# Kernel optimization log

Hardware: AMD Instinct MI355X
Metric: run time of the kernel (lower is better)

## Reference

```python
import jax, jax.numpy as jnp
import numpy as np

LOG_EPS = 1e-30
MIN_EPS = 1e-8
N_CLASS = 19
GAMMA = 1.0        # focal_gamma
ADAPT_B = 0.2
ADAPT_A = 0.9      # beta (a_decay == 0)
ADAPT_D = 8.0
CONF_THRESH = 0.8  # uda_confidence_thresh


def setup_inputs() -> dict:
    key = jax.random.key(0)
    k1, k2 = jax.random.split(key)
    N, C, H, W = 2, N_CLASS, 512, 1024
    logits_before = jax.random.normal(k1, (N, C, H, W), jnp.float32)
    logits_after = jax.random.normal(k2, (N, C, H, W), jnp.float32)
    cls_thresh = jnp.ones((N_CLASS,), jnp.float32) * CONF_THRESH
    return {"logits_before": logits_before, "logits_after": logits_after,
            "cls_thresh": cls_thresh}


def ias_thresh(conf, label, cls_thresh):
    # conf, label: [N,H,W] max-prob and argmax class per pixel
    conf_f = conf.reshape(-1)    # [T]
    label_f = label.reshape(-1)  # [T]

    def per_class(c, thr):
        # class-c confidences, others pushed to the end of the descending sort
        vals = jnp.where(label_f == c, conf_f, -jnp.inf)
        ext = jnp.concatenate([vals, thr[None]])  # append current threshold
        srt = -jnp.sort(-ext)                     # descending
        count = jnp.sum(label_f == c)
        # index = int(len_extend * adapt_b * thresh**adapt_d); len_extend = count+1
        idx = jnp.floor((count + 1).astype(jnp.float32) * ADAPT_B * thr ** ADAPT_D).astype(jnp.int32)
        return srt[idx]  # count==0 -> idx==0 -> picks thr (matches torch branch)

    return jax.vmap(per_class)(jnp.arange(N_CLASS), cls_thresh)


def reference(logits_before, logits_after, cls_thresh):
    pb = jax.nn.softmax(logits_before, axis=1)
    pa = jax.nn.softmax(logits_after, axis=1)
    pb_d = jax.lax.stop_gradient(pb)
    log_pb_d = jnp.log(pb_d + LOG_EPS)
    log_pa = jnp.log(pa + LOG_EPS)

    bma = 1.0 - pa  # focal_type == 1: ones_like(pb_d) - pa
    label = jnp.argmax(pb_d, axis=1)  # [N,H,W]
    conf = jnp.max(pb_d, axis=1)      # [N,H,W]
    # scatter(select_mask)+sum == gather the argmax channel
    sel_diff = jnp.take_along_axis(bma, label[:, None], axis=1)  # [N,1,H,W]

    loss_kldiv = pb_d * (log_pb_d - jnp.abs(sel_diff) ** GAMMA * log_pa)
    loss_entropy = -pb * jnp.log(pb + LOG_EPS)
    loss = jnp.sum(loss_kldiv + loss_entropy, axis=1)  # [N,H,W]

    tmp = ias_thresh(conf, label, cls_thresh)
    new_thresh = ADAPT_A * cls_thresh + (1.0 - ADAPT_A) * tmp
    new_thresh = jnp.where(new_thresh >= 1.0, 0.999, new_thresh)

    pix_thresh = new_thresh[label]           # [N,H,W]
    mask = conf > pix_thresh
    adapt_ratio = jnp.mean(mask.astype(jnp.float32))
    solid_ratio = jnp.mean((conf > CONF_THRESH).astype(jnp.float32))

    # loss[mask] -> clamp -> mean, expressed as a masked mean (jit-safe)
    num = jnp.sum(jnp.where(mask, jnp.maximum(loss, MIN_EPS), 0.0))
    den = jnp.maximum(jnp.sum(mask).astype(loss.dtype), 1.0)
    return num / den, adapt_ratio, solid_ratio
```

## Files before the change

### kernel.cpp

```cpp
#include <hip/hip_runtime.h>
#include <math.h>

#define NCLS 19
#define HW   (512*1024)
#define CHW  (NCLS*HW)
#define TPIX (2*HW)
#define NB   512
#define NPART 32
#define CAND_MAX 4096
#define SUBB 1024
#define SCAP 256

#define WS_PART   0
#define WS_CANDC  622592
#define WS_ACCUM  622720
#define WS_DONE   622784
#define WS_SEL    622848
#define WS_NEWTH  623360
#define WS_CONF   623616
#define WS_LOSS   4817920
#define WS_LABEL  9012224
#define WS_CAND   10060800

#define CH_STRIDE4 (HW/4)
__global__ __launch_bounds__(256, 4)
void k1_pixel(const float* __restrict__ lb_t, const float* __restrict__ la_t,
              float* __restrict__ conf_o, float* __restrict__ loss_o,
              unsigned char* __restrict__ label_o,
              unsigned int* __restrict__ cand_cnt,
              unsigned int* __restrict__ accum_u,
              unsigned int* __restrict__ done)
{
    const int tid = threadIdx.x;
    if (blockIdx.x == 0) {
        if (tid < NCLS)            cand_cnt[tid] = 0u;
        else if (tid < NCLS + 3)   accum_u[tid - NCLS] = 0u;
        else if (tid < NCLS + 5)   done[tid - NCLS - 3] = 0u;
    }
    const int g    = blockIdx.x * 256 + tid;
    const int pix0 = g << 2;
    const int n    = pix0 >> 19;
    const int rem  = pix0 & (HW - 1);
    const float4* bb = (const float4*)(lb_t + (size_t)n * CHW + rem);
    const float4* ab = (const float4*)(la_t + (size_t)n * CHW + rem);

    float mb[4], zb[4], dot[4], ma[4], za[4], a_lab[4];
    int lab[4];
#pragma unroll
    for (int j = 0; j < 4; ++j) {
        mb[j] = -INFINITY; ma[j] = -INFINITY;
        zb[j] = 0.0f; za[j] = 0.0f; dot[j] = 0.0f; a_lab[j] = 0.0f; lab[j] = -1;
    }

    float4 bA0, bA1, bA2, bA3, aA0, aA1, aA2, aA3;
    float4 bB0, bB1, bB2, bB3, aB0, aB1, aB2, aB3;

#define LOADA(c0, NC)                                                          \
    do {                                                                       \
        bA0 = bb[(size_t)(c0 + 0) * CH_STRIDE4];                               \
        aA0 = ab[(size_t)(c0 + 0) * CH_STRIDE4];                               \
        if (NC > 1) { bA1 = bb[(size_t)(c0 + 1) * CH_STRIDE4];                 \
                      aA1 = ab[(size_t)(c0 + 1) * CH_STRIDE4]; }               \
        if (NC > 2) { bA2 = bb[(size_t)(c0 + 2) * CH_STRIDE4];                 \
                      aA2 = ab[(size_t)(c0 + 2) * CH_STRIDE4]; }               \
        if (NC > 3) { bA3 = bb[(size_t)(c0 + 3) * CH_STRIDE4];                 \
                      aA3 = ab[(size_t)(c0 + 3) * CH_STRIDE4]; }               \
        __builtin_amdgcn_sched_barrier(0);                                     \
    } while (0)
#define LOADB(c0, NC)                                                          \
    do {                                                                       \
        bB0 = bb[(size_t)(c0 + 0) * CH_STRIDE4];                               \
        aB0 = ab[(size_t)(c0 + 0) * CH_STRIDE4];                               \
        if (NC > 1) { bB1 = bb[(size_t)(c0 + 1) * CH_STRIDE4];                 \
                      aB1 = ab[(size_t)(c0 + 1) * CH_STRIDE4]; }               \
        if (NC > 2) { bB2 = bb[(size_t)(c0 + 2) * CH_STRIDE4];                 \
                      aB2 = ab[(size_t)(c0 + 2) * CH_STRIDE4]; }               \
        if (NC > 3) { bB3 = bb[(size_t)(c0 + 3) * CH_STRIDE4];                 \
                      aB3 = ab[(size_t)(c0 + 3) * CH_STRIDE4]; }               \
        __builtin_amdgcn_sched_barrier(0);                                     \
    } while (0)

#define STEP(c, bv, av)                                                        \
    do {                                                                       \
        _Pragma("unroll")                                                      \
        for (int j = 0; j < 4; ++j) {                                          \
            float b = ((const float*)&(bv))[j];                                \
            float a = ((const float*)&(av))[j];                                \
            float mn = fmaxf(mb[j], b);                                        \
            float eo = __expf(mb[j] - mn);       \
            float en = __expf(b - mn);                                         \
            zb[j]  = zb[j] * eo + en;                                          \
            dot[j] = dot[j] * eo + en * a;                                     \
            bool upd = b > mb[j];               \
            lab[j]   = upd ? (c) : lab[j];                                     \
            a_lab[j] = upd ? a : a_lab[j];                                     \
            mb[j] = mn;                                                        \
            float mna = fmaxf(ma[j], a);                                       \
            za[j] = za[j] * __expf(ma[j] - mna) + __expf(a - mna);             \
            ma[j] = mna;                                                       \
        }                                                                      \
    } while (0)

    LOADA(0, 4);
    LOADB(4, 4);
    STEP(0, bA0, aA0); STEP(1, bA1, aA1); STEP(2, bA2, aA2); STEP(3, bA3, aA3);
    LOADA(8, 4);
    STEP(4, bB0, aB0); STEP(5, bB1, aB1); STEP(6, bB2, aB2); STEP(7, bB3, aB3);
    LOADB(12, 4);
    STEP(8, bA0, aA0); STEP(9, bA1, aA1); STEP(10, bA2, aA2); STEP(11, bA3, aA3);
    LOADA(16, 3);
    STEP(12, bB0, aB0); STEP(13, bB1, aB1); STEP(14, bB2, aB2); STEP(15, bB3, aB3);
    STEP(16, bA0, aA0); STEP(17, bA1, aA1); STEP(18, bA2, aA2);

    float4 cf4, ls4; uchar4 lb4;
#pragma unroll
    for (int j = 0; j < 4; ++j) {
        float cf = 1.0f / zb[j];
        float pa_lab = __expf(a_lab[j] - ma[j]) / za[j];
        float ls = (1.0f - pa_lab) * (ma[j] + __logf(za[j]) - dot[j] / zb[j]);
        ((float*)&cf4)[j] = cf;
        ((float*)&ls4)[j] = ls;
        ((unsigned char*)&lb4)[j] = (unsigned char)lab[j];
    }
    ((float4*)conf_o)[g] = cf4;
    ((float4*)loss_o)[g] = ls4;
    ((uchar4*)label_o)[g] = lb4;
#undef LOADA
#undef LOADB
#undef STEP
}

__global__ __launch_bounds__(512)
void k2_hist(const float4* __restrict__ conf, const uchar4* __restrict__ label,
             unsigned short* __restrict__ part)
{
    __shared__ unsigned int lh[NCLS * NB];
    const int t = threadIdx.x;
    for (int w = t; w < NCLS * NB; w += 512) lh[w] = 0u;
    __syncthreads();

    const int per4  = TPIX / 4 / NPART;
    const int base4 = blockIdx.x * per4;
    for (int i = 0; i < per4 / 512; ++i) {
        int g = base4 + i * 512 + t;
        float4 c4 = conf[g];
        uchar4 l4 = label[g];
        float cf[4] = {c4.x, c4.y, c4.z, c4.w};
        int   lb[4] = {l4.x, l4.y, l4.z, l4.w};
#pragma unroll
        for (int k = 0; k < 4; ++k) {
            int bin = (int)(cf[k] * (float)NB);
            bin = bin < (NB - 1) ? bin : (NB - 1);
            atomicAdd(&lh[lb[k] * NB + bin], 1u);
        }
    }
    __syncthreads();

    unsigned short* dst = part + blockIdx.x * (NCLS * NB);
    for (int w = t; w < NCLS * NB; w += 512) dst[w] = (unsigned short)lh[w];
}

__global__ __launch_bounds__(256)
void k2_select(const unsigned short* __restrict__ part, const float* __restrict__ cls_thresh,
               int* __restrict__ sel, unsigned int* __restrict__ cand_cnt,
               float* __restrict__ cand)
{
    int c = blockIdx.x;
    int t = threadIdx.x;
    float thr = cls_thresh[c];
    int thr_bin = (int)(thr * (float)NB); thr_bin = thr_bin < (NB-1) ? thr_bin : (NB-1);

    int base = NB - (t + 1) * 2;
    unsigned h0 = 0, h1 = 0;
#pragma unroll 8
    for (int b = 0; b < NPART; ++b) {
        const unsigned short* p = part + b * (NCLS * NB) + c * NB;
        h0 += p[base];
        h1 += p[base + 1];
    }
    if (base == thr_bin)     h0 += 1u;
    if (base + 1 == thr_bin) h1 += 1u;
    unsigned s = h0 + h1;

    __shared__ unsigned sc[256];
    sc[t] = s;
    __syncthreads();
    for (int off = 1; off < 256; off <<= 1) {
        unsigned vt = sc[t];
        unsigned vp = (t >= off) ? sc[t - off] : 0u;
        __syncthreads();
        sc[t] = vt + vp;
        __syncthreads();
    }
    unsigned total_ext = sc[255];
    unsigned cnt = total_ext - 1u;
    int idx = (int)floorf((float)(cnt + 1u) * 0.2f * powf(thr, 8.0f));

    unsigned above = sc[t] - s;
    if ((unsigned)idx >= above && (unsigned)idx < above + s) {
        int B, r;
        if ((unsigned)idx < above + h1) { B = base + 1; r = (int)((unsigned)idx - above); }
        else                            { B = base;     r = (int)((unsigned)idx - above - h1); }
        sel[2 * c]     = B;
        sel[2 * c + 1] = r;
        if (B == thr_bin) {
            unsigned pos = atomicAdd(&cand_cnt[c], 1u);
            if (pos < CAND_MAX) cand[c * CAND_MAX + pos] = thr;
        }
    }
}

__global__ __launch_bounds__(256)
void k3_gather(const float4* __restrict__ conf, const uchar4* __restrict__ label,
               const int* __restrict__ sel, unsigned int* __restrict__ cand_cnt,
               float* __restrict__ cand)
{
    int g = blockIdx.x * 256 + threadIdx.x;
    float4 c4 = conf[g];
    uchar4 l4 = label[g];
    float cf[4] = {c4.x, c4.y, c4.z, c4.w};
    int   lb[4] = {l4.x, l4.y, l4.z, l4.w};
#pragma unroll
    for (int i = 0; i < 4; ++i) {
        int bin = (int)(cf[i] * (float)NB);
        bin = bin < (NB - 1) ? bin : (NB - 1);
        if (bin == sel[2 * lb[i]]) {
            unsigned pos = atomicAdd(&cand_cnt[lb[i]], 1u);
            if (pos < CAND_MAX) cand[lb[i] * CAND_MAX + pos] = cf[i];
        }
    }
}

__global__ __launch_bounds__(256)
void k4_thresh(const int* __restrict__ sel, const unsigned int* __restrict__ cand_cnt,
               const float* __restrict__ cand, const float* __restrict__ cls_thresh,
               float* __restrict__ newth)
{
    __shared__ unsigned int subh[SUBB];
    __shared__ float        sbuf[SCAP];
    __shared__ unsigned int scnt;
    __shared__ int          sS;
    __shared__ unsigned int sR2;
    __shared__ float        sres;

    const int c = blockIdx.x;
    const int t = threadIdx.x;
    unsigned mc = cand_cnt[c];
    int m = (int)(mc < (unsigned)CAND_MAX ? mc : (unsigned)CAND_MAX);
    int B = sel[2 * c];
    int r = sel[2 * c + 1];
    const float* v = cand + c * CAND_MAX;
    const float scale = (float)NB;

    for (int i = t; i < SUBB; i += 256) subh[i] = 0u;
    if (t == 0) { scnt = 0u; sS = 0; sR2 = 0u; sres = 0.0f; }
    __syncthreads();

    for (int i = t; i < m; i += 256) {
        float x = v[i];
        int s = (int)((x * scale - (float)B) * (float)SUBB);
        s = s < 0 ? 0 : (s > SUBB - 1 ? SUBB - 1 : s);
        atomicAdd(&subh[s], 1u);
    }
    __syncthreads();

    if (t < 64) {
        int lane = t;
        int cb = SUBB - 16 * (lane + 1);
        unsigned hsum = 0;
        for (int i = 0; i < 16; ++i) hsum += subh[cb + i];
        unsigned incl = hsum;
        for (int off = 1; off < 64; off <<= 1) {
            unsigned q = __shfl_up(incl, off, 64);
            if (lane >= off) incl += q;
        }
        unsigned above = incl - hsum;
        if ((unsigned)r >= above && (unsigned)r < above + hsum) {
            unsigned cum = above;
            for (int i = 15; i >= 0; --i) {
                unsigned h = subh[cb + i];
                if ((unsigned)r < cum + h) { sS = cb + i; sR2 = (unsigned)r - cum; break; }
                cum += h;
            }
        }
    }
    __syncthreads();
    const int S = sS;
    const unsigned r2 = sR2;

    for (int i = t; i < m; i += 256) {
        float x = v[i];
        int s = (int)((x * scale - (float)B) * (float)SUBB);
        s = s < 0 ? 0 : (s > SUBB - 1 ? SUBB - 1 : s);
        if (s == S) {
            unsigned p = atomicAdd(&scnt, 1u);
            if (p < (unsigned)SCAP) sbuf[p] = x;
        }
    }
    __syncthreads();
    unsigned cntS = scnt;

    if (cntS <= (unsigned)SCAP) {
        for (int i = t; i < (int)cntS; i += 256) {
            float x = sbuf[i];
            int gc = 0, e = 0;
            for (int j = 0; j < (int)cntS; ++j) {
                float y = sbuf[j];
                gc += (y > x); e += (y == x);
            }
            if (gc <= (int)r2 && (int)r2 < gc + e) sres = x;
        }
    } else {
        for (int i = t; i < m; i += 256) {
            float x = v[i];
            int s = (int)((x * scale - (float)B) * (float)SUBB);
            s = s < 0 ? 0 : (s > SUBB - 1 ? SUBB - 1 : s);
            if (s != S) continue;
            int gc = 0, e = 0;
            for (int j = 0; j < m; ++j) {
                float y = v[j];
                int sj = (int)((y * scale - (float)B) * (float)SUBB);
                sj = sj < 0 ? 0 : (sj > SUBB - 1 ? SUBB - 1 : sj);
                if (sj != S) continue;
                gc += (y > x); e += (y == x);
            }
            if (gc <= (int)r2 && (int)r2 < gc + e) sres = x;
        }
    }
    __syncthreads();
    if (t == 0) {
        float thr = cls_thresh[c];
        float nt = 0.9f * thr + 0.1f * sres;
        if (nt >= 1.0f) nt = 0.999f;
        newth[c] = nt;
    }
}

__global__ __launch_bounds__(256)
void k5_reduce_out(const float4* __restrict__ conf, const float4* __restrict__ loss,
                   const uchar4* __restrict__ label, const float* __restrict__ newth,
                   float* __restrict__ accum, unsigned int* __restrict__ done,
                   float* __restrict__ out)
{
    __shared__ float th[NCLS];
    if (threadIdx.x < NCLS) th[threadIdx.x] = newth[threadIdx.x];
    __syncthreads();

    int g = blockIdx.x * 256 + threadIdx.x;
    float4 c4 = conf[g];
    float4 s4 = loss[g];
    uchar4 l4 = label[g];
    float cf[4] = {c4.x, c4.y, c4.z, c4.w};
    float lv[4] = {s4.x, s4.y, s4.z, s4.w};
    int   lb[4] = {l4.x, l4.y, l4.z, l4.w};

    float ls = 0.0f; int mask = 0, solid = 0;
#pragma unroll
    for (int i = 0; i < 4; ++i) {
        bool m = cf[i] > th[lb[i]];
        mask  += m ? 1 : 0;
        solid += (cf[i] > 0.8f) ? 1 : 0;
        ls    += m ? fmaxf(lv[i], 1e-8f) : 0.0f;
    }
    for (int off = 32; off > 0; off >>= 1) {
        ls    += __shfl_down(ls, off, 64);
        mask  += __shfl_down(mask, off, 64);
        solid += __shfl_down(solid, off, 64);
    }
    __shared__ float s_ls[4];
    __shared__ int   s_m[4], s_s[4];
    int w = threadIdx.x >> 6;
    if ((threadIdx.x & 63) == 0) { s_ls[w] = ls; s_m[w] = mask; s_s[w] = solid; }
    __syncthreads();
    __shared__ int s_last;
    if (threadIdx.x == 0) {
        float L = s_ls[0] + s_ls[1] + s_ls[2] + s_ls[3];
        int   M = s_m[0] + s_m[1] + s_m[2] + s_m[3];
        int   S = s_s[0] + s_s[1] + s_s[2] + s_s[3];
        atomicAdd(&accum[0], L);
        atomicAdd(&((unsigned int*)accum)[1], (unsigned)M);
        atomicAdd(&((unsigned int*)accum)[2], (unsigned)S);
        __threadfence();
        s_last = (atomicAdd(&done[0], 1u) == (unsigned)(gridDim.x - 1)) ? 1 : 0;
    }
    __syncthreads();
    if (!s_last) return;
    if (threadIdx.x == 0) {
        __threadfence();
        float sum = accum[0];
        unsigned cm = ((const unsigned int*)accum)[1];
        unsigned cs = ((const unsigned int*)accum)[2];
        out[0] = sum / fmaxf((float)cm, 1.0f);
        out[1] = (float)cm / (float)TPIX;
        out[2] = (float)cs / (float)TPIX;
    }
}

extern "C" void kernel_launch(void* const* d_in, const int* in_sizes, int n_in,
                              void* d_out, int out_size, void* d_ws, size_t ws_size,
                              hipStream_t stream)
{
    const float* lb  = (const float*)d_in[0];
    const float* la  = (const float*)d_in[1];
    const float* cth = (const float*)d_in[2];
    float* out = (float*)d_out;

    char* ws = (char*)d_ws;
    unsigned short* part     = (unsigned short*)(ws + WS_PART);
    unsigned int*   cand_cnt = (unsigned int*)(ws + WS_CANDC);
    float*          accum    = (float*)(ws + WS_ACCUM);
    unsigned int*   done     = (unsigned int*)(ws + WS_DONE);
    int*            sel      = (int*)(ws + WS_SEL);
    float*          newth    = (float*)(ws + WS_NEWTH);
    float*          conf     = (float*)(ws + WS_CONF);
    float*          loss     = (float*)(ws + WS_LOSS);
    unsigned char*  label    = (unsigned char*)(ws + WS_LABEL);
    float*          cand     = (float*)(ws + WS_CAND);

    dim3 grd1(TPIX / 4 / 256);
    dim3 grd4(TPIX / 4 / 256);

    k1_pixel<<<grd1, dim3(256), 0, stream>>>(lb, la, conf, loss, label,
                                             cand_cnt, (unsigned int*)accum, done);
    k2_hist<<<NPART, dim3(512), 0, stream>>>((const float4*)conf, (const uchar4*)label, part);
    k2_select<<<NCLS, dim3(256), 0, stream>>>(part, cth, sel, cand_cnt, cand);
    k3_gather<<<grd4, dim3(256), 0, stream>>>((const float4*)conf, (const uchar4*)label,
                                              sel, cand_cnt, cand);
    k4_thresh<<<NCLS, dim3(256), 0, stream>>>(sel, cand_cnt, cand, cth, newth);
    k5_reduce_out<<<grd4, dim3(256), 0, stream>>>((const float4*)conf, (const float4*)loss,
                                                  (const uchar4*)label, newth, accum, done, out);
}
```

Measured before the change: 251.0 us.

## Fuse histogram, select, gather, threshold and reduce into one persistent kernel

```diff
diff --git a/kernel.cpp b/kernel.cpp
--- a/kernel.cpp
+++ b/kernel.cpp
@@ -10,11 +10,12 @@
 #define CAND_MAX 4096
 #define SUBB 1024
 #define SCAP 256
+#define GRID_CO 256
 
 #define WS_PART   0
 #define WS_CANDC  622592
 #define WS_ACCUM  622720
-#define WS_DONE   622784
+#define WS_BAR    622784
 #define WS_SEL    622848
 #define WS_NEWTH  623360
 #define WS_CONF   623616
@@ -29,13 +30,13 @@
               unsigned char* __restrict__ label_o,
               unsigned int* __restrict__ cand_cnt,
               unsigned int* __restrict__ accum_u,
-              unsigned int* __restrict__ done)
+              unsigned int* __restrict__ bar)
 {
     const int tid = threadIdx.x;
     if (blockIdx.x == 0) {
-        if (tid < NCLS)            cand_cnt[tid] = 0u;
-        else if (tid < NCLS + 3)   accum_u[tid - NCLS] = 0u;
-        else if (tid < NCLS + 5)   done[tid - NCLS - 3] = 0u;
+        if (tid < NCLS)             cand_cnt[tid] = 0u;
+        else if (tid < NCLS + 3)    accum_u[tid - NCLS] = 0u;
+        else if (tid < NCLS + 11)   bar[tid - NCLS - 3] = 0u;
     }
     const int g    = blockIdx.x * 256 + tid;
     const int pix0 = g << 2;
@@ -79,7 +80,6 @@
                       aB3 = ab[(size_t)(c0 + 3) * CH_STRIDE4]; }               \
         __builtin_amdgcn_sched_barrier(0);                                     \
     } while (0)
-
 #define STEP(c, bv, av)                                                        \
     do {                                                                       \
         _Pragma("unroll")                                                      \
@@ -130,266 +130,268 @@
 #undef STEP
 }
 
-__global__ __launch_bounds__(512)
-void k2_hist(const float4* __restrict__ conf, const uchar4* __restrict__ label,
-             unsigned short* __restrict__ part)
+__device__ __forceinline__ void grid_barrier(unsigned int* cnt, unsigned nb)
 {
-    __shared__ unsigned int lh[NCLS * NB];
+    __threadfence();
+    __syncthreads();
+    if (threadIdx.x == 0) {
+        atomicAdd(cnt, 1u);
+        int it = 0;
+        while (atomicAdd(cnt, 0u) < nb && it < (1 << 20)) {
+            __builtin_amdgcn_s_sleep(8);
+            ++it;
+        }
+    }
+    __syncthreads();
+    __threadfence();
+}
+
+__global__ __launch_bounds__(256, 2)
+void k2_fused(const float4* __restrict__ conf4, const float4* __restrict__ loss4,
+              const uchar4* __restrict__ label4,
+              unsigned short* __restrict__ part, const float* __restrict__ cls_thresh,
+              int* __restrict__ sel, unsigned int* __restrict__ cand_cnt,
+              float* __restrict__ cand, float* __restrict__ newth,
+              float* __restrict__ accum, unsigned int* __restrict__ bar,
+              float* __restrict__ out)
+{
+    __shared__ unsigned int shm[NCLS * NB];
     const int t = threadIdx.x;
-    for (int w = t; w < NCLS * NB; w += 512) lh[w] = 0u;
-    __syncthreads();
-
-    const int per4  = TPIX / 4 / NPART;
-    const int base4 = blockIdx.x * per4;
-    for (int i = 0; i < per4 / 512; ++i) {
-        int g = base4 + i * 512 + t;
-        float4 c4 = conf[g];
-        uchar4 l4 = label[g];
+    const int b = blockIdx.x;
+    const unsigned nb = gridDim.x;
+
+    if (b < NPART) {
+        for (int w = t; w < NCLS * NB; w += 256) shm[w] = 0u;
+        __syncthreads();
+        const int per4  = TPIX / 4 / NPART;
+        const int base4 = b * per4;
+        for (int i = 0; i < per4 / 256; ++i) {
+            int g = base4 + i * 256 + t;
+            float4 c4 = conf4[g];
+            uchar4 l4 = label4[g];
+            float cf[4] = {c4.x, c4.y, c4.z, c4.w};
+            int   lb[4] = {l4.x, l4.y, l4.z, l4.w};
+#pragma unroll
+            for (int k = 0; k < 4; ++k) {
+                int bin = (int)(cf[k] * (float)NB);
+                bin = bin < (NB - 1) ? bin : (NB - 1);
+                atomicAdd(&shm[lb[k] * NB + bin], 1u);
+            }
+        }
+        __syncthreads();
+        unsigned short* dst = part + b * (NCLS * NB);
+        for (int w = t; w < NCLS * NB; w += 256) dst[w] = (unsigned short)shm[w];
+    }
+    grid_barrier(&bar[0], nb);
+
+    if (b < NCLS) {
+        const int c = b;
+        unsigned* sc = shm;
+        float thr = cls_thresh[c];
+        int thr_bin = (int)(thr * (float)NB); thr_bin = thr_bin < (NB-1) ? thr_bin : (NB-1);
+        int base = NB - (t + 1) * 2;
+        unsigned h0 = 0, h1 = 0;
+#pragma unroll 8
+        for (int p = 0; p < NPART; ++p) {
+            const unsigned short* pp = part + p * (NCLS * NB) + c * NB;
+            h0 += pp[base];
+            h1 += pp[base + 1];
+        }
+        if (base == thr_bin)     h0 += 1u;
+        if (base + 1 == thr_bin) h1 += 1u;
+        unsigned s = h0 + h1;
+        sc[t] = s;
+        __syncthreads();
+        for (int off = 1; off < 256; off <<= 1) {
+            unsigned vt = sc[t];
+            unsigned vp = (t >= off) ? sc[t - off] : 0u;
+            __syncthreads();
+            sc[t] = vt + vp;
+            __syncthreads();
+        }
+        unsigned total_ext = sc[255];
+        unsigned cnt = total_ext - 1u;
+        int idx = (int)floorf((float)(cnt + 1u) * 0.2f * powf(thr, 8.0f));
+        unsigned above = sc[t] - s;
+        if ((unsigned)idx >= above && (unsigned)idx < above + s) {
+            int B, r;
+            if ((unsigned)idx < above + h1) { B = base + 1; r = (int)((unsigned)idx - above); }
+            else                            { B = base;     r = (int)((unsigned)idx - above - h1); }
+            sel[2 * c]     = B;
+            sel[2 * c + 1] = r;
+            if (B == thr_bin) {
+                unsigned pos = atomicAdd(&cand_cnt[c], 1u);
+                if (pos < CAND_MAX) cand[c * CAND_MAX + pos] = thr;
+            }
+        }
+    }
+    grid_barrier(&bar[1], nb);
+
+    for (int g = b * 256 + t; g < TPIX / 4; g += GRID_CO * 256) {
+        float4 c4 = conf4[g];
+        uchar4 l4 = label4[g];
         float cf[4] = {c4.x, c4.y, c4.z, c4.w};
         int   lb[4] = {l4.x, l4.y, l4.z, l4.w};
 #pragma unroll
-        for (int k = 0; k < 4; ++k) {
-            int bin = (int)(cf[k] * (float)NB);
+        for (int i = 0; i < 4; ++i) {
+            int bin = (int)(cf[i] * (float)NB);
             bin = bin < (NB - 1) ? bin : (NB - 1);
-            atomicAdd(&lh[lb[k] * NB + bin], 1u);
-        }
-    }
-    __syncthreads();
-
-    unsigned short* dst = part + blockIdx.x * (NCLS * NB);
-    for (int w = t; w < NCLS * NB; w += 512) dst[w] = (unsigned short)lh[w];
-}
-
-__global__ __launch_bounds__(256)
-void k2_select(const unsigned short* __restrict__ part, const float* __restrict__ cls_thresh,
-               int* __restrict__ sel, unsigned int* __restrict__ cand_cnt,
-               float* __restrict__ cand)
-{
-    int c = blockIdx.x;
-    int t = threadIdx.x;
-    float thr = cls_thresh[c];
-    int thr_bin = (int)(thr * (float)NB); thr_bin = thr_bin < (NB-1) ? thr_bin : (NB-1);
-
-    int base = NB - (t + 1) * 2;
-    unsigned h0 = 0, h1 = 0;
-#pragma unroll 8
-    for (int b = 0; b < NPART; ++b) {
-        const unsigned short* p = part + b * (NCLS * NB) + c * NB;
-        h0 += p[base];
-        h1 += p[base + 1];
-    }
-    if (base == thr_bin)     h0 += 1u;
-    if (base + 1 == thr_bin) h1 += 1u;
-    unsigned s = h0 + h1;
-
-    __shared__ unsigned sc[256];
-    sc[t] = s;
-    __syncthreads();
-    for (int off = 1; off < 256; off <<= 1) {
-        unsigned vt = sc[t];
-        unsigned vp = (t >= off) ? sc[t - off] : 0u;
-        __syncthreads();
-        sc[t] = vt + vp;
-        __syncthreads();
-    }
-    unsigned total_ext = sc[255];
-    unsigned cnt = total_ext - 1u;
-    int idx = (int)floorf((float)(cnt + 1u) * 0.2f * powf(thr, 8.0f));
-
-    unsigned above = sc[t] - s;
-    if ((unsigned)idx >= above && (unsigned)idx < above + s) {
-        int B, r;
-        if ((unsigned)idx < above + h1) { B = base + 1; r = (int)((unsigned)idx - above); }
-        else                            { B = base;     r = (int)((unsigned)idx - above - h1); }
-        sel[2 * c]     = B;
-        sel[2 * c + 1] = r;
-        if (B == thr_bin) {
-            unsigned pos = atomicAdd(&cand_cnt[c], 1u);
-            if (pos < CAND_MAX) cand[c * CAND_MAX + pos] = thr;
-        }
-    }
-}
-
-__global__ __launch_bounds__(256)
-void k3_gather(const float4* __restrict__ conf, const uchar4* __restrict__ label,
-               const int* __restrict__ sel, unsigned int* __restrict__ cand_cnt,
-               float* __restrict__ cand)
-{
-    int g = blockIdx.x * 256 + threadIdx.x;
-    float4 c4 = conf[g];
-    uchar4 l4 = label[g];
-    float cf[4] = {c4.x, c4.y, c4.z, c4.w};
-    int   lb[4] = {l4.x, l4.y, l4.z, l4.w};
-#pragma unroll
-    for (int i = 0; i < 4; ++i) {
-        int bin = (int)(cf[i] * (float)NB);
-        bin = bin < (NB - 1) ? bin : (NB - 1);
-        if (bin == sel[2 * lb[i]]) {
-            unsigned pos = atomicAdd(&cand_cnt[lb[i]], 1u);
-            if (pos < CAND_MAX) cand[lb[i] * CAND_MAX + pos] = cf[i];
-        }
-    }
-}
-
-__global__ __launch_bounds__(256)
-void k4_thresh(const int* __restrict__ sel, const unsigned int* __restrict__ cand_cnt,
-               const float* __restrict__ cand, const float* __restrict__ cls_thresh,
-               float* __restrict__ newth)
-{
-    __shared__ unsigned int subh[SUBB];
-    __shared__ float        sbuf[SCAP];
-    __shared__ unsigned int scnt;
-    __shared__ int          sS;
-    __shared__ unsigned int sR2;
-    __shared__ float        sres;
-
-    const int c = blockIdx.x;
-    const int t = threadIdx.x;
-    unsigned mc = cand_cnt[c];
-    int m = (int)(mc < (unsigned)CAND_MAX ? mc : (unsigned)CAND_MAX);
-    int B = sel[2 * c];
-    int r = sel[2 * c + 1];
-    const float* v = cand + c * CAND_MAX;
-    const float scale = (float)NB;
-
-    for (int i = t; i < SUBB; i += 256) subh[i] = 0u;
-    if (t == 0) { scnt = 0u; sS = 0; sR2 = 0u; sres = 0.0f; }
-    __syncthreads();
-
-    for (int i = t; i < m; i += 256) {
-        float x = v[i];
-        int s = (int)((x * scale - (float)B) * (float)SUBB);
-        s = s < 0 ? 0 : (s > SUBB - 1 ? SUBB - 1 : s);
-        atomicAdd(&subh[s], 1u);
-    }
-    __syncthreads();
-
-    if (t < 64) {
-        int lane = t;
-        int cb = SUBB - 16 * (lane + 1);
-        unsigned hsum = 0;
-        for (int i = 0; i < 16; ++i) hsum += subh[cb + i];
-        unsigned incl = hsum;
-        for (int off = 1; off < 64; off <<= 1) {
-            unsigned q = __shfl_up(incl, off, 64);
-            if (lane >= off) incl += q;
-        }
-        unsigned above = incl - hsum;
-        if ((unsigned)r >= above && (unsigned)r < above + hsum) {
-            unsigned cum = above;
-            for (int i = 15; i >= 0; --i) {
-                unsigned h = subh[cb + i];
-                if ((unsigned)r < cum + h) { sS = cb + i; sR2 = (unsigned)r - cum; break; }
-                cum += h;
-            }
-        }
-    }
-    __syncthreads();
-    const int S = sS;
-    const unsigned r2 = sR2;
-
-    for (int i = t; i < m; i += 256) {
-        float x = v[i];
-        int s = (int)((x * scale - (float)B) * (float)SUBB);
-        s = s < 0 ? 0 : (s > SUBB - 1 ? SUBB - 1 : s);
-        if (s == S) {
-            unsigned p = atomicAdd(&scnt, 1u);
-            if (p < (unsigned)SCAP) sbuf[p] = x;
-        }
-    }
-    __syncthreads();
-    unsigned cntS = scnt;
-
-    if (cntS <= (unsigned)SCAP) {
-        for (int i = t; i < (int)cntS; i += 256) {
-            float x = sbuf[i];
-            int gc = 0, e = 0;
-            for (int j = 0; j < (int)cntS; ++j) {
-                float y = sbuf[j];
-                gc += (y > x); e += (y == x);
-            }
-            if (gc <= (int)r2 && (int)r2 < gc + e) sres = x;
-        }
-    } else {
+            if (bin == sel[2 * lb[i]]) {
+                unsigned pos = atomicAdd(&cand_cnt[lb[i]], 1u);
+                if (pos < CAND_MAX) cand[lb[i] * CAND_MAX + pos] = cf[i];
+            }
+        }
+    }
+    grid_barrier(&bar[2], nb);
+
+    if (b < NCLS) {
+        const int c = b;
+        unsigned int* subh = shm;
+        unsigned int* scnt = shm + SUBB;
+        int*          sS   = (int*)(shm + SUBB + 1);
+        unsigned int* sR2  = shm + SUBB + 2;
+        float*        sres = (float*)(shm + SUBB + 3);
+        float*        sbuf = (float*)(shm + SUBB + 4);
+
+        unsigned mc = cand_cnt[c];
+        int m = (int)(mc < (unsigned)CAND_MAX ? mc : (unsigned)CAND_MAX);
+        int B = sel[2 * c];
+        int r = sel[2 * c + 1];
+        const float* v = cand + c * CAND_MAX;
+        const float scale = (float)NB;
+
+        for (int i = t; i < SUBB; i += 256) subh[i] = 0u;
+        if (t == 0) { *scnt = 0u; *sS = 0; *sR2 = 0u; *sres = 0.0f; }
+        __syncthreads();
+
         for (int i = t; i < m; i += 256) {
             float x = v[i];
             int s = (int)((x * scale - (float)B) * (float)SUBB);
             s = s < 0 ? 0 : (s > SUBB - 1 ? SUBB - 1 : s);
-            if (s != S) continue;
-            int gc = 0, e = 0;
-            for (int j = 0; j < m; ++j) {
-                float y = v[j];
-                int sj = (int)((y * scale - (float)B) * (float)SUBB);
-                sj = sj < 0 ? 0 : (sj > SUBB - 1 ? SUBB - 1 : sj);
-                if (sj != S) continue;
-                gc += (y > x); e += (y == x);
-            }
-            if (gc <= (int)r2 && (int)r2 < gc + e) sres = x;
-        }
-    }
-    __syncthreads();
-    if (t == 0) {
-        float thr = cls_thresh[c];
-        float nt = 0.9f * thr + 0.1f * sres;
-        if (nt >= 1.0f) nt = 0.999f;
-        newth[c] = nt;
-    }
-}
-
-__global__ __launch_bounds__(256)
-void k5_reduce_out(const float4* __restrict__ conf, const float4* __restrict__ loss,
-                   const uchar4* __restrict__ label, const float* __restrict__ newth,
-                   float* __restrict__ accum, unsigned int* __restrict__ done,
-                   float* __restrict__ out)
-{
-    __shared__ float th[NCLS];
-    if (threadIdx.x < NCLS) th[threadIdx.x] = newth[threadIdx.x];
-    __syncthreads();
-
-    int g = blockIdx.x * 256 + threadIdx.x;
-    float4 c4 = conf[g];
-    float4 s4 = loss[g];
-    uchar4 l4 = label[g];
-    float cf[4] = {c4.x, c4.y, c4.z, c4.w};
-    float lv[4] = {s4.x, s4.y, s4.z, s4.w};
-    int   lb[4] = {l4.x, l4.y, l4.z, l4.w};
-
-    float ls = 0.0f; int mask = 0, solid = 0;
+            atomicAdd(&subh[s], 1u);
+        }
+        __syncthreads();
+
+        if (t < 64) {
+            int lane = t;
+            int cb = SUBB - 16 * (lane + 1);
+            unsigned hsum = 0;
+            for (int i = 0; i < 16; ++i) hsum += subh[cb + i];
+            unsigned incl = hsum;
+            for (int off = 1; off < 64; off <<= 1) {
+                unsigned q = __shfl_up(incl, off, 64);
+                if (lane >= off) incl += q;
+            }
+            unsigned above = incl - hsum;
+            if ((unsigned)r >= above && (unsigned)r < above + hsum) {
+                unsigned cum = above;
+                for (int i = 15; i >= 0; --i) {
+                    unsigned h = subh[cb + i];
+                    if ((unsigned)r < cum + h) { *sS = cb + i; *sR2 = (unsigned)r - cum; break; }
+                    cum += h;
+                }
+            }
+        }
+        __syncthreads();
+        const int S = *sS;
+        const unsigned r2 = *sR2;
+
+        for (int i = t; i < m; i += 256) {
+            float x = v[i];
+            int s = (int)((x * scale - (float)B) * (float)SUBB);
+            s = s < 0 ? 0 : (s > SUBB - 1 ? SUBB - 1 : s);
+            if (s == S) {
+                unsigned p = atomicAdd(scnt, 1u);
+                if (p < (unsigned)SCAP) sbuf[p] = x;
+            }
+        }
+        __syncthreads();
+        unsigned cntS = *scnt;
+
+        if (cntS <= (unsigned)SCAP) {
+            for (int i = t; i < (int)cntS; i += 256) {
+                float x = sbuf[i];
+                int gc = 0, e = 0;
+                for (int j = 0; j < (int)cntS; ++j) {
+                    float y = sbuf[j];
+                    gc += (y > x); e += (y == x);
+                }
+                if (gc <= (int)r2 && (int)r2 < gc + e) *sres = x;
+            }
+        } else {
+            for (int i = t; i < m; i += 256) {
+                float x = v[i];
+                int s = (int)((x * scale - (float)B) * (float)SUBB);
+                s = s < 0 ? 0 : (s > SUBB - 1 ? SUBB - 1 : s);
+                if (s != S) continue;
+                int gc = 0, e = 0;
+                for (int j = 0; j < m; ++j) {
+                    float y = v[j];
+                    int sj = (int)((y * scale - (float)B) * (float)SUBB);
+                    sj = sj < 0 ? 0 : (sj > SUBB - 1 ? SUBB - 1 : sj);
+                    if (sj != S) continue;
+                    gc += (y > x); e += (y == x);
+                }
+                if (gc <= (int)r2 && (int)r2 < gc + e) *sres = x;
+            }
+        }
+        __syncthreads();
+        if (t == 0) {
+            float thr = cls_thresh[c];
+            float nt = 0.9f * thr + 0.1f * (*sres);
+            if (nt >= 1.0f) nt = 0.999f;
+            newth[c] = nt;
+        }
+    }
+    grid_barrier(&bar[3], nb);
+
+    {
+        float* th   = (float*)shm;
+        float* s_ls = (float*)(shm + 32);
+        int*   s_m  = (int*)(shm + 36);
+        int*   s_s  = (int*)(shm + 40);
+        if (t < NCLS) th[t] = newth[t];
+        __syncthreads();
+
+        float ls = 0.0f; int mask = 0, solid = 0;
+        for (int g = b * 256 + t; g < TPIX / 4; g += GRID_CO * 256) {
+            float4 c4 = conf4[g];
+            float4 s4 = loss4[g];
+            uchar4 l4 = label4[g];
+            float cf[4] = {c4.x, c4.y, c4.z, c4.w};
+            float lv[4] = {s4.x, s4.y, s4.z, s4.w};
+            int   lb[4] = {l4.x, l4.y, l4.z, l4.w};
 #pragma unroll
-    for (int i = 0; i < 4; ++i) {
-        bool m = cf[i] > th[lb[i]];
-        mask  += m ? 1 : 0;
-        solid += (cf[i] > 0.8f) ? 1 : 0;
-        ls    += m ? fmaxf(lv[i], 1e-8f) : 0.0f;
-    }
-    for (int off = 32; off > 0; off >>= 1) {
-        ls    += __shfl_down(ls, off, 64);
-        mask  += __shfl_down(mask, off, 64);
-        solid += __shfl_down(solid, off, 64);
-    }
-    __shared__ float s_ls[4];
-    __shared__ int   s_m[4], s_s[4];
-    int w = threadIdx.x >> 6;
-    if ((threadIdx.x & 63) == 0) { s_ls[w] = ls; s_m[w] = mask; s_s[w] = solid; }
-    __syncthreads();
-    __shared__ int s_last;
-    if (threadIdx.x == 0) {
-        float L = s_ls[0] + s_ls[1] + s_ls[2] + s_ls[3];
-        int   M = s_m[0] + s_m[1] + s_m[2] + s_m[3];
-        int   S = s_s[0] + s_s[1] + s_s[2] + s_s[3];
-        atomicAdd(&accum[0], L);
-        atomicAdd(&((unsigned int*)accum)[1], (unsigned)M);
-        atomicAdd(&((unsigned int*)accum)[2], (unsigned)S);
-        __threadfence();
-        s_last = (atomicAdd(&done[0], 1u) == (unsigned)(gridDim.x - 1)) ? 1 : 0;
-    }
-    __syncthreads();
-    if (!s_last) return;
-    if (threadIdx.x == 0) {
-        __threadfence();
-        float sum = accum[0];
-        unsigned cm = ((const unsigned int*)accum)[1];
-        unsigned cs = ((const unsigned int*)accum)[2];
+            for (int i = 0; i < 4; ++i) {
+                bool m = cf[i] > th[lb[i]];
+                mask  += m ? 1 : 0;
+                solid += (cf[i] > 0.8f) ? 1 : 0;
+                ls    += m ? fmaxf(lv[i], 1e-8f) : 0.0f;
+            }
+        }
+        for (int off = 32; off > 0; off >>= 1) {
+            ls    += __shfl_down(ls, off, 64);
+            mask  += __shfl_down(mask, off, 64);
+            solid += __shfl_down(solid, off, 64);
+        }
+        int w = t >> 6;
+        if ((t & 63) == 0) { s_ls[w] = ls; s_m[w] = mask; s_s[w] = solid; }
+        __syncthreads();
+        if (t == 0) {
+            float L = s_ls[0] + s_ls[1] + s_ls[2] + s_ls[3];
+            int   M = s_m[0] + s_m[1] + s_m[2] + s_m[3];
+            int   S = s_s[0] + s_s[1] + s_s[2] + s_s[3];
+            atomicAdd(&accum[0], L);
+            atomicAdd(&((unsigned int*)accum)[1], (unsigned)M);
+            atomicAdd(&((unsigned int*)accum)[2], (unsigned)S);
+        }
+    }
+    grid_barrier(&bar[4], nb);
+
+    if (b == 0 && t == 0) {
+        float sum   = atomicAdd(&accum[0], 0.0f);
+        unsigned cm = atomicAdd(&((unsigned int*)accum)[1], 0u);
+        unsigned cs = atomicAdd(&((unsigned int*)accum)[2], 0u);
         out[0] = sum / fmaxf((float)cm, 1.0f);
         out[1] = (float)cm / (float)TPIX;
         out[2] = (float)cs / (float)TPIX;
@@ -409,7 +411,7 @@
     unsigned short* part     = (unsigned short*)(ws + WS_PART);
     unsigned int*   cand_cnt = (unsigned int*)(ws + WS_CANDC);
     float*          accum    = (float*)(ws + WS_ACCUM);
-    unsigned int*   done     = (unsigned int*)(ws + WS_DONE);
+    unsigned int*   bar      = (unsigned int*)(ws + WS_BAR);
     int*            sel      = (int*)(ws + WS_SEL);
     float*          newth    = (float*)(ws + WS_NEWTH);
     float*          conf     = (float*)(ws + WS_CONF);
@@ -418,15 +420,10 @@
     float*          cand     = (float*)(ws + WS_CAND);
 
     dim3 grd1(TPIX / 4 / 256);
-    dim3 grd4(TPIX / 4 / 256);
 
     k1_pixel<<<grd1, dim3(256), 0, stream>>>(lb, la, conf, loss, label,
-                                             cand_cnt, (unsigned int*)accum, done);
-    k2_hist<<<NPART, dim3(512), 0, stream>>>((const float4*)conf, (const uchar4*)label, part);
-    k2_select<<<NCLS, dim3(256), 0, stream>>>(part, cth, sel, cand_cnt, cand);
-    k3_gather<<<grd4, dim3(256), 0, stream>>>((const float4*)conf, (const uchar4*)label,
-                                              sel, cand_cnt, cand);
-    k4_thresh<<<NCLS, dim3(256), 0, stream>>>(sel, cand_cnt, cand, cth, newth);
-    k5_reduce_out<<<grd4, dim3(256), 0, stream>>>((const float4*)conf, (const float4*)loss,
-                                                  (const uchar4*)label, newth, accum, done, out);
+                                             cand_cnt, (unsigned int*)accum, bar);
+    k2_fused<<<dim3(GRID_CO), dim3(256), 0, stream>>>(
+        (const float4*)conf, (const float4*)loss, (const uchar4*)label,
+        part, cth, sel, cand_cnt, cand, newth, accum, bar, out);
 }
```

Result: slower. 394.7 us (+57.2%).
